# Performance work log

Hardware: AMD Instinct MI355X
Metric: run time of the kernel (lower is better)

Reference implementation:

```python
import jax, jax.numpy as jnp
import numpy as np

B, S, D, H = 1, 2048, 4096, 32
HD = D // H  # 128


def setup_inputs() -> dict:
    key = jax.random.key(0)
    ks = jax.random.split(key, 6)
    x = jax.random.normal(ks[0], (B, S, D), dtype=jnp.float32)
    # rotary angles: standard llama freqs, position * inv_freq
    inv_freq = 1.0 / (10000.0 ** (jnp.arange(0, HD, 2, dtype=jnp.float32) / HD))  # (HD/2,)
    freqs = jnp.arange(S, dtype=jnp.float32)[:, None] * inv_freq[None, :]  # (S, HD/2)
    scale = 0.02
    wq = jax.random.normal(ks[1], (D, D), dtype=jnp.float32) * scale
    wk = jax.random.normal(ks[2], (D, D), dtype=jnp.float32) * scale
    wv = jax.random.normal(ks[3], (D, D), dtype=jnp.float32) * scale
    wo = jax.random.normal(ks[4], (D, D), dtype=jnp.float32) * scale
    return {"x": x, "freqs": freqs, "wq": wq, "wk": wk, "wv": wv, "wo": wo}


def _rope(t, cos, sin):
    # t: (B,S,H,HD); pairs are interleaved (complex view of last dim)
    b, s, h, d = t.shape
    t2 = t.reshape(b, s, h, d // 2, 2)
    t0, t1 = t2[..., 0], t2[..., 1]
    o0 = t0 * cos - t1 * sin
    o1 = t0 * sin + t1 * cos
    return jnp.stack([o0, o1], axis=-1).reshape(b, s, h, d)


def reference(x, freqs, wq, wk, wv, wo):
    b, s, d = x.shape
    hd = 2 * freqs.shape[-1]
    h = d // hd
    # projections (torch Linear: y = x @ W.T)
    q = (x @ wq.T).reshape(b, s, h, hd)
    k = (x @ wk.T).reshape(b, s, h, hd)
    v = (x @ wv.T).reshape(b, s, h, hd)
    cos = jnp.cos(freqs)[None, :s, None, :]  # (1,S,1,HD/2)
    sin = jnp.sin(freqs)[None, :s, None, :]
    q = _rope(q, cos, sin)
    k = _rope(k, cos, sin)
    q = q.transpose(0, 2, 1, 3)  # (B,H,S,HD)
    k = k.transpose(0, 2, 1, 3)
    v = v.transpose(0, 2, 1, 3)
    scale = jnp.sqrt(jnp.float32(hd))
    scores = jnp.einsum('bhqd,bhkd->bhqk', q, k).astype(jnp.float32) / scale
    # causal mask (qp == ep path): -inf strictly above diagonal
    mask = jnp.triu(jnp.full((s, s), -jnp.inf, dtype=scores.dtype), k=1)
    scores = scores + mask[None, None]
    attn = jax.nn.softmax(scores, axis=-1).astype(q.dtype)
    out = jnp.einsum('bhqk,bhkd->bhqd', attn, v)
    out = out.transpose(0, 2, 1, 3).reshape(b, s, d)
    return out @ wo.T
```

## Files before the change

### kernel.cpp

```cpp
#include <hip/hip_runtime.h>
#include <hip/hip_bf16.h>
#include <stdint.h>


typedef __attribute__((ext_vector_type(8))) short bf16x8;
typedef __attribute__((ext_vector_type(4))) float f32x4;

#define S_LEN 2048
#define DMODEL 4096
#define NHEAD 32
#define HDIM 128
#define QKV_LD 12288

#define QSCALE 0.1275247584969759f

__device__ __forceinline__ unsigned short f2bf(float f) {
  unsigned int u = __float_as_uint(f);
  unsigned int r = u + 0x7FFFu + ((u >> 16) & 1u);
  return (unsigned short)(r >> 16);
}
__device__ __forceinline__ float bf2f(unsigned short h) {
  return __uint_as_float(((unsigned int)h) << 16);
}
__device__ __forceinline__ void gl_lds16(const void* g, void* l) {
  __builtin_amdgcn_global_load_lds((const __attribute__((address_space(1))) unsigned int*)g,
                                   (__attribute__((address_space(3))) unsigned int*)l, 16, 0, 0);
}
__device__ __forceinline__ void phase_barrier() {
  __builtin_amdgcn_sched_barrier(0);
  asm volatile("" ::: "memory");
  __builtin_amdgcn_s_barrier();
  asm volatile("" ::: "memory");
  __builtin_amdgcn_sched_barrier(0);
}
__device__ __forceinline__ void wait_vmcnt6() {
  __builtin_amdgcn_sched_barrier(0);
  asm volatile("s_waitcnt vmcnt(6)" ::: "memory");
  __builtin_amdgcn_sched_barrier(0);
}
__device__ __forceinline__ void wait_vmcnt4() {
  __builtin_amdgcn_sched_barrier(0);
  asm volatile("s_waitcnt vmcnt(4)" ::: "memory");
  __builtin_amdgcn_sched_barrier(0);
}

__device__ __forceinline__ void cvt4(const float* __restrict__ s, unsigned short* __restrict__ d,
                                     int i) {
  float4 v = ((const float4*)s)[i];
  ushort4 o;
  o.x = f2bf(v.x); o.y = f2bf(v.y); o.z = f2bf(v.z); o.w = f2bf(v.w);
  ((ushort4*)d)[i] = o;
}

__global__ __launch_bounds__(256) void prep_inputs(const float* __restrict__ x,
                                                   const float* __restrict__ wq,
                                                   const float* __restrict__ wk,
                                                   const float* __restrict__ wv,
                                                   const float* __restrict__ wo,
                                                   const float* __restrict__ fr,
                                                   unsigned short* __restrict__ xb,
                                                   unsigned short* __restrict__ wqkvb,
                                                   unsigned short* __restrict__ wob,
                                                   float* __restrict__ cs) {
  const int NX = 2097152;
  const int NW = 4194304;
  const int NR = S_LEN * 64;
  const int total = NX + 4 * NW + NR;
  int i = blockIdx.x * blockDim.x + threadIdx.x;
  int stride = gridDim.x * blockDim.x;
  for (; i < total; i += stride) {
    if (i < NX) {
      cvt4(x, xb, i);
    } else if (i < NX + NW) {
      cvt4(wq, wqkvb, i - NX);
    } else if (i < NX + 2 * NW) {
      cvt4(wk, wqkvb + 16777216, i - NX - NW);
    } else if (i < NX + 3 * NW) {
      cvt4(wv, wqkvb + 33554432, i - NX - 2 * NW);
    } else if (i < NX + 4 * NW) {
      cvt4(wo, wob, i - NX - 3 * NW);
    } else {
      int j = i - (NX + 4 * NW);
      float f = fr[j];
      cs[2 * j]     = cosf(f);
      cs[2 * j + 1] = sinf(f);
    }
  }
}

__device__ __forceinline__ void mfma_quad(f32x4 (&acc)[8][4], const bf16x8 (&af)[4][2],
                                          const bf16x8 (&bf)[2][2], int moff, int noff) {
  __builtin_amdgcn_s_setprio(1);
#pragma unroll
  for (int mi = 0; mi < 4; ++mi)
#pragma unroll
    for (int ni = 0; ni < 2; ++ni)
#pragma unroll
      for (int kk = 0; kk < 2; ++kk)
        acc[moff + mi][noff + ni] = __builtin_amdgcn_mfma_f32_16x16x32_bf16(
            af[mi][kk], bf[ni][kk], acc[moff + mi][noff + ni], 0, 0, 0);
  __builtin_amdgcn_s_setprio(0);
}
__device__ __forceinline__ void mfma_quad2(f32x4 (&acc)[4][4], const bf16x8 (&af)[2][2],
                                           const bf16x8 (&bf)[2][2], int moff, int noff) {
  __builtin_amdgcn_s_setprio(1);
#pragma unroll
  for (int mi = 0; mi < 2; ++mi)
#pragma unroll
    for (int ni = 0; ni < 2; ++ni)
#pragma unroll
      for (int kk = 0; kk < 2; ++kk)
        acc[moff + mi][noff + ni] = __builtin_amdgcn_mfma_f32_16x16x32_bf16(
            af[mi][kk], bf[ni][kk], acc[moff + mi][noff + ni], 0, 0, 0);
  __builtin_amdgcn_s_setprio(0);
}

__device__ __forceinline__ void read_a(bf16x8 (&dst)[4][2], const char* base, int half,
                                       int wr, int l15, int l4, int swz) {
#pragma unroll
  for (int mi = 0; mi < 4; ++mi) {
    const char* rb = base + (wr * 128 + half * 64 + mi * 16 + l15) * 128;
#pragma unroll
    for (int kk = 0; kk < 2; ++kk)
      dst[mi][kk] = *(const bf16x8*)(rb + ((kk * 64 + l4 * 16) ^ swz));
  }
}
__device__ __forceinline__ void read_b(bf16x8 (&dst)[2][2], const char* base, int half,
                                       int wc, int l15, int l4, int swz) {
#pragma unroll
  for (int ni = 0; ni < 2; ++ni) {
    const char* rb = base + (wc * 64 + half * 32 + ni * 16 + l15) * 128;
#pragma unroll
    for (int kk = 0; kk < 2; ++kk)
      dst[ni][kk] = *(const bf16x8*)(rb + ((kk * 64 + l4 * 16) ^ swz));
  }
}
__device__ __forceinline__ void read_a2(bf16x8 (&dst)[2][2], const char* base, int half,
                                        int wr, int l15, int l4, int swz) {
#pragma unroll
  for (int mi = 0; mi < 2; ++mi) {
    const char* rb = base + (wr * 64 + half * 32 + mi * 16 + l15) * 128;
#pragma unroll
    for (int kk = 0; kk < 2; ++kk)
      dst[mi][kk] = *(const bf16x8*)(rb + ((kk * 64 + l4 * 16) ^ swz));
  }
}
__device__ __forceinline__ void read_b2(bf16x8 (&dst)[2][2], const char* base, int half,
                                        int wc, int l15, int l4, int swz) {
#pragma unroll
  for (int ni = 0; ni < 2; ++ni) {
    const char* rb = base + (wc * 64 + half * 32 + ni * 16 + l15) * 128;
#pragma unroll
    for (int kk = 0; kk < 2; ++kk)
      dst[ni][kk] = *(const bf16x8*)(rb + ((kk * 64 + l4 * 16) ^ swz));
  }
}

template <bool OUT_BF16, bool ROPE>
__device__ __forceinline__ void gemm256_body(const unsigned short* __restrict__ A,
                                             const unsigned short* __restrict__ B,
                                             void* __restrict__ C,
                                             int M, int N, int K, int ldc,
                                             char* smem, int wg,
                                             const float* __restrict__ cs) {
  const int tid = threadIdx.x;
  const int lane = tid & 63, wid = tid >> 6;
  const int wr = wid >> 2, wc = wid & 3;
  const int l15 = lane & 15, l4 = lane >> 4;

  const int nbn = N >> 8;
  const int bm = wg / nbn, bn = wg % nbn;
  const int nk = K >> 6;

  unsigned short* AlB = (unsigned short*)smem;
  unsigned short* BlB = (unsigned short*)smem + 32768;

  const int srow = tid >> 3;
  const int scol = ((tid & 7) ^ (srow & 7)) * 8;
  const unsigned short* Asrc = A + (size_t)(bm * 256 + srow) * K + scol;
  const unsigned short* Bsrc = B + (size_t)(bn * 256 + srow) * K + scol;
  const int ldsdst = wid * 512;

#define STA(b, kt, q) gl_lds16(Asrc + ((size_t)(q) * 64) * K + (kt) * 64, AlB + (b) * 16384 + (q) * 4096 + ldsdst)
#define STB(b, kt, q) gl_lds16(Bsrc + ((size_t)(q) * 64) * K + (kt) * 64, BlB + (b) * 16384 + (q) * 4096 + ldsdst)

  const int swz = (l15 & 7) << 4;

  f32x4 acc[8][4] = {};
  bf16x8 Ax[4][2], Ay[4][2], B0f[2][2], B1f[2][2];

#pragma unroll
  for (int q = 0; q < 4; ++q) STA(0, 0, q);
#pragma unroll
  for (int q = 0; q < 4; ++q) STB(0, 0, q);
  {
    const int k1 = (nk > 1) ? 1 : 0;
    STA(1, k1, 0); STA(1, k1, 2);
    STB(1, k1, 0); STB(1, k1, 1); STB(1, k1, 2); STB(1, k1, 3);
  }
  wait_vmcnt6();
  phase_barrier();
  read_a(Ax, (const char*)AlB, 0, wr, l15, l4, swz);
  read_b(B0f, (const char*)BlB, 0, wc, l15, l4, swz);

#define HALF(bb, AC, AA, t)                                                \
  {                                                                        \
    const int kt1 = ((t) + 1 < nk) ? (t) + 1 : nk - 1;                     \
    const int kt2 = ((t) + 2 < nk) ? (t) + 2 : nk - 1;                     \
    const char* Ab = (const char*)(AlB + (bb) * 16384);                    \
    const char* Bb = (const char*)(BlB + (bb) * 16384);                    \
    const char* Abn = (const char*)(AlB + ((bb) ^ 1) * 16384);             \
    const char* Bbn = (const char*)(BlB + ((bb) ^ 1) * 16384);             \
    STA((bb) ^ 1, kt1, 1); STA((bb) ^ 1, kt1, 3);                          \
    phase_barrier();                                                       \
    mfma_quad(acc, AC, B0f, 0, 0);                                 \
    read_a(AA, Ab, 1, wr, l15, l4, swz);                                   \
    STA(bb, kt2, 0); STA(bb, kt2, 2);                                      \
    phase_barrier();                                                       \
    mfma_quad(acc, AA, B0f, 4, 0);                                 \
    read_b(B1f, Bb, 1, wc, l15, l4, swz);                                  \
    STB(bb, kt2, 0); STB(bb, kt2, 1);                                      \
    phase_barrier();                                                       \
    mfma_quad(acc, AA, B1f, 4, 2);                                 \
    STB(bb, kt2, 2); STB(bb, kt2, 3);                                      \
    wait_vmcnt6();                                                         \
    phase_barrier();                                                       \
    mfma_quad(acc, AC, B1f, 0, 2);                                 \
    read_a(AA, Abn, 0, wr, l15, l4, swz);                                  \
    read_b(B0f, Bbn, 0, wc, l15, l4, swz);                                 \
  }

  for (int t = 0; t < nk; t += 2) {
    HALF(0, Ax, Ay, t);
    HALF(1, Ay, Ax, t + 1);
  }
#undef HALF
#undef STA
#undef STB

  __builtin_amdgcn_sched_barrier(0);
  asm volatile("s_waitcnt vmcnt(0)" ::: "memory");

  const size_t crow0 = (size_t)bm * 256 + wr * 128 + l4 * 4;
  const int ccol0 = bn * 256 + wc * 64 + l15;
#pragma unroll
  for (int mf = 0; mf < 8; ++mf)
#pragma unroll
    for (int nf = 0; nf < 4; ++nf) {
      size_t row = crow0 + mf * 16;
      int col = ccol0 + nf * 16;
      if (ROPE) {
        const int d = col & (HDIM - 1);
        const int i2 = d & ~1;
        const float fs = (col < 4096) ? QSCALE : 1.0f;
        unsigned short* Cp = (unsigned short*)C;
#pragma unroll
        for (int r = 0; r < 4; ++r) {
          float v = acc[mf][nf][r];
          float vp = __shfl_xor(v, 1, 64);
          float2 csv = *(const float2*)&cs[(row + r) * HDIM + i2];
          float o = ((d & 1) == 0) ? (v * csv.x - vp * csv.y)
                                   : (vp * csv.y + v * csv.x);
          Cp[(row + r) * ldc + col] = f2bf(o * fs);
        }
      } else if (OUT_BF16) {
        unsigned short* Cp = (unsigned short*)C;
#pragma unroll
        for (int r = 0; r < 4; ++r) Cp[(row + r) * ldc + col] = f2bf(acc[mf][nf][r]);
      } else {
        float* Cp = (float*)C;
#pragma unroll
        for (int r = 0; r < 4; ++r) Cp[(row + r) * ldc + col] = acc[mf][nf][r];
      }
    }
}

template <bool OUT_BF16, bool VT_OUT>
__device__ __forceinline__ void gemm128_body(const unsigned short* __restrict__ A,
                                             const unsigned short* __restrict__ B,
                                             void* __restrict__ C,
                                             int M, int N, int K, int ldc,
                                             char* smem, int wg) {
  const int tid = threadIdx.x;
  const int lane = tid & 63, wid = tid >> 6;
  const int wr = wid >> 2, wc = wid & 3;
  const int l15 = lane & 15, l4 = lane >> 4;

  const int nbn = N >> 8;
  const int bm = wg / nbn, bn = wg % nbn;
  const int nk = K >> 6;

  unsigned short* AlB = (unsigned short*)smem;
  unsigned short* BlB = (unsigned short*)smem + 16384;

  const int srow = tid >> 3;
  const int scol = ((tid & 7) ^ (srow & 7)) * 8;
  const unsigned short* Asrc = A + (size_t)(bm * 128 + srow) * K + scol;
  const unsigned short* Bsrc = B + (size_t)(bn * 256 + srow) * K + scol;
  const int ldsdst = wid * 512;

#define STA2(b, kt, q) gl_lds16(Asrc + ((size_t)(q) * 64) * K + (kt) * 64, AlB + (b) * 8192 + (q) * 4096 + ldsdst)
#define STB2(b, kt, q) gl_lds16(Bsrc + ((size_t)(q) * 64) * K + (kt) * 64, BlB + (b) * 16384 + (q) * 4096 + ldsdst)

  const int swz = (l15 & 7) << 4;

  f32x4 acc[4][4] = {};
  bf16x8 Ax[2][2], Ay[2][2], B0f[2][2], B1f[2][2];

  STA2(0, 0, 0); STA2(0, 0, 1);
#pragma unroll
  for (int q = 0; q < 4; ++q) STB2(0, 0, q);
  {
    const int k1 = (nk > 1) ? 1 : 0;
    STA2(1, k1, 0); STA2(1, k1, 1);
    STB2(1, k1, 0); STB2(1, k1, 1);
  }
  wait_vmcnt4();
  phase_barrier();
  read_a2(Ax, (const char*)AlB, 0, wr, l15, l4, swz);
  read_b2(B0f, (const char*)BlB, 0, wc, l15, l4, swz);

#define HALF2(bb, AC, AA, t)                                               \
  {                                                                        \
    const int kt1 = ((t) + 1 < nk) ? (t) + 1 : nk - 1;                     \
    const int kt2 = ((t) + 2 < nk) ? (t) + 2 : nk - 1;                     \
    const char* Ab = (const char*)(AlB + (bb) * 8192);                     \
    const char* Bb = (const char*)(BlB + (bb) * 16384);                    \
    const char* Abn = (const char*)(AlB + ((bb) ^ 1) * 8192);              \
    const char* Bbn = (const char*)(BlB + ((bb) ^ 1) * 16384);             \
    STB2((bb) ^ 1, kt1, 2); STB2((bb) ^ 1, kt1, 3);        \
    phase_barrier();                                                       \
    mfma_quad2(acc, AC, B0f, 0, 0);                                \
    read_a2(AA, Ab, 1, wr, l15, l4, swz);                                  \
    STA2(bb, kt2, 0); STA2(bb, kt2, 1);                                    \
    phase_barrier();                                                       \
    mfma_quad2(acc, AA, B0f, 2, 0);                                \
    read_b2(B1f, Bb, 1, wc, l15, l4, swz);                                 \
    STB2(bb, kt2, 0); STB2(bb, kt2, 1);                                    \
    phase_barrier();                                                       \
    mfma_quad2(acc, AA, B1f, 2, 2);                                \
    wait_vmcnt4();                                                         \
    phase_barrier();                                                       \
    mfma_quad2(acc, AC, B1f, 0, 2);                                \
    read_a2(AA, Abn, 0, wr, l15, l4, swz);                                 \
    read_b2(B0f, Bbn, 0, wc, l15, l4, swz);                                \
  }

  for (int t = 0; t < nk; t += 2) {
    HALF2(0, Ax, Ay, t);
    HALF2(1, Ay, Ax, t + 1);
  }
#undef HALF2
#undef STA2
#undef STB2

  __builtin_amdgcn_sched_barrier(0);
  asm volatile("s_waitcnt vmcnt(0)" ::: "memory");

  if (VT_OUT) {
    unsigned short* Tw = (unsigned short*)smem + (size_t)wid * 4672;
#pragma unroll
    for (int mf = 0; mf < 4; ++mf)
#pragma unroll
      for (int nf = 0; nf < 4; ++nf)
#pragma unroll
        for (int r = 0; r < 4; ++r) {
          int lr = mf * 16 + l4 * 4 + r;
          int lc = nf * 16 + l15;
          Tw[lr * 73 + lc] = f2bf(acc[mf][nf][r]);
        }
    __syncthreads();
    unsigned short* vtp = (unsigned short*)C;
    const int gcol0 = bn * 256 + wc * 64;
    const int grow0 = bm * 128 + wr * 64;
    const int dl8 = lane >> 3, sc = lane & 7;
#pragma unroll
    for (int it = 0; it < 8; ++it) {
      int dl = it * 8 + dl8;
      unsigned short tmp[8];
#pragma unroll
      for (int j = 0; j < 8; ++j) tmp[j] = Tw[(sc * 8 + j) * 73 + dl];
      unsigned short* dst = vtp + (size_t)(gcol0 + dl) * S_LEN + grow0 + sc * 8;
      *(ushort4*)dst = make_ushort4(tmp[0], tmp[1], tmp[2], tmp[3]);
      *(ushort4*)(dst + 4) = make_ushort4(tmp[4], tmp[5], tmp[6], tmp[7]);
    }
    return;
  }

  const size_t crow0 = (size_t)bm * 128 + wr * 64 + l4 * 4;
  const int ccol0 = bn * 256 + wc * 64 + l15;
#pragma unroll
  for (int mf = 0; mf < 4; ++mf)
#pragma unroll
    for (int nf = 0; nf < 4; ++nf) {
      size_t row = crow0 + mf * 16;
      int col = ccol0 + nf * 16;
      if (OUT_BF16) {
        unsigned short* Cp = (unsigned short*)C;
#pragma unroll
        for (int r = 0; r < 4; ++r) Cp[(row + r) * ldc + col] = f2bf(acc[mf][nf][r]);
      } else {
        float* Cp = (float*)C;
#pragma unroll
        for (int r = 0; r < 4; ++r) Cp[(row + r) * ldc + col] = acc[mf][nf][r];
      }
    }
}

__global__ __launch_bounds__(512, 2) void qkv_proj(const unsigned short* __restrict__ xb,
                                                   const unsigned short* __restrict__ wqkvb,
                                                   unsigned short* __restrict__ qkvb,
                                                   unsigned short* __restrict__ vt,
                                                   const float* __restrict__ cs) {
  __shared__ __align__(16) char smem[131072];
  const int b = blockIdx.x;
  if (b < 256) {
    gemm256_body<true, true>(xb, wqkvb, qkvb, 2048, 8192, 4096, QKV_LD, smem, b, cs);
  } else {
    gemm128_body<true, true>(xb, wqkvb + 33554432, vt, 2048, 4096, 4096, 0, smem, b - 256);
  }
}

__global__ __launch_bounds__(512, 2) void out_proj(const unsigned short* __restrict__ A,
                                                   const unsigned short* __restrict__ B,
                                                   float* __restrict__ C) {
  __shared__ __align__(16) char smem[98304];
  gemm128_body<false, false>(A, B, C, 2048, 4096, 4096, 4096, smem, blockIdx.x);
}

__global__ __launch_bounds__(256) void attn_kernel(const unsigned short* __restrict__ qkv,
                                                   const unsigned short* __restrict__ vt,
                                                   float* __restrict__ pacc,
                                                   float* __restrict__ pm,
                                                   float* __restrict__ pl,
                                                   unsigned short* __restrict__ out) {
  __shared__ __align__(16) unsigned short Klds[64 * 128];
  __shared__ __align__(16) unsigned short Vtlds[128 * 64];
  __shared__ __align__(16) unsigned short Plds[4][16 * 64];
  const int tid = threadIdx.x, lane = tid & 63, w = tid >> 6;
  const int l15 = lane & 15, l4 = lane >> 4;
  const int h = blockIdx.x & 31;
  const int jj = blockIdx.x >> 5;

  int bq, c, kt0, kt1;
  if (jj < 17) {
    bq = 31 - jj; c = 0; kt0 = 0; kt1 = 16;
  } else {
    int k = jj - 17;
    if (k == 0)      { bq = 31;            c = 1; }
    else if (k & 1)  { bq = 30 - (k >> 1); c = 1; }
    else             { bq = 15 - (k >> 1); c = 0; }
    kt0 = c ? 16 : 0;
    kt1 = bq + 1;
  }
  if (jj == 16) kt1 = 16;
  const int qw = bq * 64 + w * 16;

  bf16x8 qf[4];
#pragma unroll
  for (int ds = 0; ds < 4; ++ds)
    qf[ds] = *(const bf16x8*)&qkv[(size_t)(qw + l15) * QKV_LD + h * HDIM + ds * 32 + l4 * 8];

  f32x4 acc[8] = {};
  float m_run[4], l_run[4];
#pragma unroll
  for (int r = 0; r < 4; ++r) { m_run[r] = -1e30f; l_run[r] = 0.f; }

  for (int kt = kt0; kt < kt1; ++kt) {
    const int kv0 = kt * 64;
    __syncthreads();
#pragma unroll
    for (int i = 0; i < 4; ++i) {
      int b = (w * 4 + i) * 64 + lane;
      int r = b >> 4, cc = b & 15;
      gl_lds16(qkv + (size_t)(kv0 + r) * QKV_LD + 4096 + h * HDIM + ((cc ^ (r & 15)) * 8),
               &Klds[(w * 4 + i) * 512]);
    }
#pragma unroll
    for (int i = 0; i < 4; ++i) {
      int b = (w * 4 + i) * 64 + lane;
      int r = b >> 3, cc = b & 7;
      gl_lds16(vt + (size_t)(h * HDIM + r) * S_LEN + kv0 + ((cc ^ (r & 7)) * 8),
               &Vtlds[(w * 4 + i) * 512]);
    }
    __syncthreads();

    f32x4 s[4] = {};
#pragma unroll
    for (int jt = 0; jt < 4; ++jt) {
      int kr = jt * 16 + l15;
#pragma unroll
      for (int ds = 0; ds < 4; ++ds) {
        int cc = (ds * 4 + l4) ^ (kr & 15);
        bf16x8 kf = *(const bf16x8*)&Klds[kr * 128 + cc * 8];
        s[jt] = __builtin_amdgcn_mfma_f32_16x16x32_bf16(qf[ds], kf, s[jt], 0, 0, 0);
      }
    }

    const bool diag = (kt == bq);
    if (diag) {
#pragma unroll
      for (int jt = 0; jt < 4; ++jt)
#pragma unroll
        for (int r = 0; r < 4; ++r) {
          int kvg = kv0 + jt * 16 + l15;
          int qg = qw + l4 * 4 + r;
          if (kvg > qg) s[jt][r] = -1e30f;
        }
    }

    float alpha[4];
#pragma unroll
    for (int r = 0; r < 4; ++r) {
      float mx = fmaxf(fmaxf(s[0][r], s[1][r]), fmaxf(s[2][r], s[3][r]));
#pragma unroll
      for (int off = 1; off < 16; off <<= 1) mx = fmaxf(mx, __shfl_xor(mx, off, 64));
      float mi = fmaxf(m_run[r], mx);
      alpha[r] = exp2f(m_run[r] - mi);
      m_run[r] = mi;
      float sum = 0.f;
#pragma unroll
      for (int jt = 0; jt < 4; ++jt) {
        float p = exp2f(s[jt][r] - mi);
        s[jt][r] = p;
        sum += p;
      }
#pragma unroll
      for (int off = 1; off < 16; off <<= 1) sum += __shfl_xor(sum, off, 64);
      l_run[r] = l_run[r] * alpha[r] + sum;
    }
#pragma unroll
    for (int dt = 0; dt < 8; ++dt)
#pragma unroll
      for (int r = 0; r < 4; ++r) acc[dt][r] *= alpha[r];

    unsigned short* P = &Plds[w][0];
#pragma unroll
    for (int jt = 0; jt < 4; ++jt)
#pragma unroll
      for (int r = 0; r < 4; ++r) {
        int row = l4 * 4 + r, col = jt * 16 + l15;
        P[(row * 64 + col) ^ ((row & 7) << 3)] = f2bf(s[jt][r]);
      }

#pragma unroll
    for (int ks = 0; ks < 2; ++ks) {
      bf16x8 pa = *(const bf16x8*)&P[(l15 * 64 + ks * 32 + l4 * 8) ^ ((l15 & 7) << 3)];
#pragma unroll
      for (int dt = 0; dt < 8; ++dt) {
        int vr = dt * 16 + l15;
        int cc = (ks * 4 + l4) ^ (vr & 7);
        bf16x8 vf = *(const bf16x8*)&Vtlds[vr * 64 + cc * 8];
        acc[dt] = __builtin_amdgcn_mfma_f32_16x16x32_bf16(pa, vf, acc[dt], 0, 0, 0);
      }
    }
  }

  if (bq < 16) {
    float inv[4];
#pragma unroll
    for (int r = 0; r < 4; ++r) inv[r] = 1.f / l_run[r];
#pragma unroll
    for (int dt = 0; dt < 8; ++dt)
#pragma unroll
      for (int r = 0; r < 4; ++r) {
        int row = qw + l4 * 4 + r;
        int col = h * HDIM + dt * 16 + l15;
        out[(size_t)row * DMODEL + col] = f2bf(acc[dt][r] * inv[r]);
      }
  } else {
    const size_t bj = ((size_t)h * 32 + bq) * 2 + c;
    float* pa = pacc + bj * 8192 + (size_t)(w * 16) * 128;
#pragma unroll
    for (int dt = 0; dt < 8; ++dt)
#pragma unroll
      for (int r = 0; r < 4; ++r)
        pa[(l4 * 4 + r) * 128 + dt * 16 + l15] = acc[dt][r];
    if (l15 == 0) {
#pragma unroll
      for (int r = 0; r < 4; ++r) {
        pm[bj * 64 + w * 16 + l4 * 4 + r] = m_run[r];
        pl[bj * 64 + w * 16 + l4 * 4 + r] = l_run[r];
      }
    }
  }
}

__global__ __launch_bounds__(256) void attn_combine(const float* __restrict__ pacc,
                                                    const float* __restrict__ pm,
                                                    const float* __restrict__ pl,
                                                    unsigned short* __restrict__ out) {
  const int x = blockIdx.x;
  const int bq = 16 + (x >> 5), h = x & 31;
  const int tid = threadIdx.x;
  const int row = tid >> 2;
  const int d0 = (tid & 3) * 32;
  const size_t base = ((size_t)h * 32 + bq) * 2;
  const float m0 = pm[base * 64 + row];
  const float l0 = pl[base * 64 + row];
  float m1 = pm[(base + 1) * 64 + row];
  float l1 = pl[(base + 1) * 64 + row];
  float M = fmaxf(m0, m1);
  float w0 = exp2f(m0 - M);
  float w1 = exp2f(m1 - M);
  float denom = w0 * l0 + w1 * l1;
  const float inv = 1.f / denom;
  const float* a0 = pacc + base * 8192 + row * 128 + d0;
  const float* a1 = a0 + 8192;
  unsigned short* op = out + (size_t)(bq * 64 + row) * DMODEL + h * HDIM + d0;
#pragma unroll
  for (int i = 0; i < 8; ++i) {
    float4 v = *(const float4*)(a0 + i * 4);
    float4 u = *(const float4*)(a1 + i * 4);
    ushort4 o;
    o.x = f2bf((w0 * v.x + w1 * u.x) * inv);
    o.y = f2bf((w0 * v.y + w1 * u.y) * inv);
    o.z = f2bf((w0 * v.z + w1 * u.z) * inv);
    o.w = f2bf((w0 * v.w + w1 * u.w) * inv);
    *(ushort4*)(op + i * 4) = o;
  }
}

extern "C" void kernel_launch(void* const* d_in, const int* in_sizes, int n_in,
                              void* d_out, int out_size, void* d_ws, size_t ws_size,
                              hipStream_t stream) {
  const float* x = (const float*)d_in[0];
  const float* fr = (const float*)d_in[1];
  const float* wq = (const float*)d_in[2];
  const float* wk = (const float*)d_in[3];
  const float* wv = (const float*)d_in[4];
  const float* wo = (const float*)d_in[5];

  char* ws = (char*)d_ws;
  const size_t OFF_XB   = 0;
  const size_t OFF_WQKV = 16777216;
  const size_t OFF_WO   = OFF_WQKV + 100663296;
  const size_t OFF_QKV  = OFF_WO + 33554432;
  const size_t OFF_CS   = OFF_QKV + 50331648;
  const size_t OFF_VT   = OFF_CS + 1048576;
  const size_t OFF_ATTN = OFF_VT + 16777216;

  unsigned short* xb    = (unsigned short*)(ws + OFF_XB);
  unsigned short* wqkvb = (unsigned short*)(ws + OFF_WQKV);
  unsigned short* wob   = (unsigned short*)(ws + OFF_WO);
  unsigned short* qkvb  = (unsigned short*)(ws + OFF_QKV);
  float*          cs    = (float*)(ws + OFF_CS);
  unsigned short* vt    = (unsigned short*)(ws + OFF_VT);
  unsigned short* attn  = (unsigned short*)(ws + OFF_ATTN);
  float* pacc = (float*)(ws + OFF_WQKV);
  float* pm   = (float*)(ws + OFF_WQKV + 67108864);
  float* pl   = (float*)(ws + OFF_WQKV + 67633152);

  prep_inputs<<<2048, 256, 0, stream>>>(x, wq, wk, wv, wo, fr, xb, wqkvb, wob, cs);
  qkv_proj<<<dim3(512), 512, 0, stream>>>(xb, wqkvb, qkvb, vt, cs);
  attn_kernel<<<dim3(1536), 256, 0, stream>>>(qkvb, vt, pacc, pm, pl, attn);
  attn_combine<<<dim3(512), 256, 0, stream>>>(pacc, pm, pl, attn);
  out_proj<<<dim3(256), 512, 0, stream>>>(attn, wob, (float*)d_out);
}
```

Measured before the change: 414.4 us.

## Prefetch next K/V tiles into LDS while computing current attention tile

Splits the K and V LDS staging so the next tile's K is loaded after QK^T finishes and the next V after PV finishes. Uses vmcnt waits plus barriers instead of a full sync-load-sync per iteration. This overlaps global-to-LDS transfers with MFMA work in the flash-attention loop. It adds extra barriers per iteration and a redundant reload on the final iteration.

```diff
diff --git a/kernel.cpp b/kernel.cpp
--- a/kernel.cpp
+++ b/kernel.cpp
@@ -466,24 +466,37 @@
 #pragma unroll
   for (int r = 0; r < 4; ++r) { m_run[r] = -1e30f; l_run[r] = 0.f; }
 
+#define STAGE_K(kt)                                                                 \
+  {                                                                                 \
+    const int kv0s = (kt) * 64;                                                     \
+    _Pragma("unroll") for (int i = 0; i < 4; ++i) {                                 \
+      int b2 = (w * 4 + i) * 64 + lane;                                             \
+      int r = b2 >> 4, cc = b2 & 15;                                                \
+      gl_lds16(qkv + (size_t)(kv0s + r) * QKV_LD + 4096 + h * HDIM +                \
+                   ((cc ^ (r & 15)) * 8),                                           \
+               &Klds[(w * 4 + i) * 512]);                                           \
+    }                                                                               \
+  }
+#define STAGE_V(kt)                                                                 \
+  {                                                                                 \
+    const int kv0s = (kt) * 64;                                                     \
+    _Pragma("unroll") for (int i = 0; i < 4; ++i) {                                 \
+      int b2 = (w * 4 + i) * 64 + lane;                                             \
+      int r = b2 >> 3, cc = b2 & 7;                                                 \
+      gl_lds16(vt + (size_t)(h * HDIM + r) * S_LEN + kv0s + ((cc ^ (r & 7)) * 8),   \
+               &Vtlds[(w * 4 + i) * 512]);                                          \
+    }                                                                               \
+  }
+
+  STAGE_K(kt0);
+  STAGE_V(kt0);
+
   for (int kt = kt0; kt < kt1; ++kt) {
     const int kv0 = kt * 64;
-    __syncthreads();
-#pragma unroll
-    for (int i = 0; i < 4; ++i) {
-      int b = (w * 4 + i) * 64 + lane;
-      int r = b >> 4, cc = b & 15;
-      gl_lds16(qkv + (size_t)(kv0 + r) * QKV_LD + 4096 + h * HDIM + ((cc ^ (r & 15)) * 8),
-               &Klds[(w * 4 + i) * 512]);
-    }
-#pragma unroll
-    for (int i = 0; i < 4; ++i) {
-      int b = (w * 4 + i) * 64 + lane;
-      int r = b >> 3, cc = b & 7;
-      gl_lds16(vt + (size_t)(h * HDIM + r) * S_LEN + kv0 + ((cc ^ (r & 7)) * 8),
-               &Vtlds[(w * 4 + i) * 512]);
-    }
-    __syncthreads();
+    const int tn = (kt + 1 < kt1) ? kt + 1 : kt1 - 1;
+
+    wait_vmcnt4();
+    phase_barrier();
 
     f32x4 s[4] = {};
 #pragma unroll
@@ -496,6 +509,9 @@
         s[jt] = __builtin_amdgcn_mfma_f32_16x16x32_bf16(qf[ds], kf, s[jt], 0, 0, 0);
       }
     }
+
+    phase_barrier();
+    STAGE_K(tn);
 
     const bool diag = (kt == bq);
     if (diag) {
@@ -543,6 +559,9 @@
         P[(row * 64 + col) ^ ((row & 7) << 3)] = f2bf(s[jt][r]);
       }
 
+    wait_vmcnt4();
+    phase_barrier();
+
 #pragma unroll
     for (int ks = 0; ks < 2; ++ks) {
       bf16x8 pa = *(const bf16x8*)&P[(l15 * 64 + ks * 32 + l4 * 8) ^ ((l15 & 7) << 3)];
@@ -554,7 +573,12 @@
         acc[dt] = __builtin_amdgcn_mfma_f32_16x16x32_bf16(pa, vf, acc[dt], 0, 0, 0);
       }
     }
-  }
+
+    phase_barrier();
+    STAGE_V(tn);
+  }
+#undef STAGE_K
+#undef STAGE_V
 
   if (bq < 16) {
     float inv[4];
```

New measurement: 420.8 us. Within noise of the previous version (+1.6%).
